# Optimization experiments

Measured on AMD Instinct MI355X. Metric: run time of the kernel, lower is better.

## Reference

```python
import jax, jax.numpy as jnp
import numpy as np

GAMMA = 1000.0


def setup_inputs() -> dict:
    key = jax.random.key(0)
    k1, k2, k3 = jax.random.split(key, 3)
    B, R, N = 4, 2048, 256  # N = n_vars + 1
    x = jax.random.normal(k1, (B, R, N), dtype=jnp.float32)
    f = jax.random.uniform(k2, (B, R, N), dtype=jnp.float32)
    y = jax.random.normal(k3, (B, R, 1), dtype=jnp.float32)
    return {"x": x, "f": f, "y": y}


def reference(x, f, y):
    # Faithful port of RLSE.forward in training mode.
    # theta is updated FIRST (with the old S), then S is updated; both are
    # divided by gamma each step, exactly as in the torch source.
    B, R, N = x.shape
    A = (x * f).reshape(B * R, N)          # coefficient rows, scanned sequentially
    b = y.reshape(B * R)                   # rhs scalars

    def step(carry, inp):
        S, theta = carry                   # S: (N,N), theta: (N,)
        a, bi = inp                        # a: (N,), bi: scalar
        # theta_computation: e = b - a.theta ; theta <- (theta + S a * e)/gamma
        e = bi - jnp.dot(a, theta)
        theta_new = (theta + (S @ a) * e) / GAMMA
        # S_computation (note the 'ii'/'kk' einsum labels take DIAGONALS of S):
        # x1[i,k] = S[i,i] * (a.a) * S[k,k] ; x2[i] = 1 + S[i,i] * (a.a)
        d = jnp.diagonal(S)                # (N,)
        s2 = jnp.dot(a, a)                 # scalar a^T a
        x2 = 1.0 + d * s2                  # (N,), broadcast over columns
        S_new = (S - (d[:, None] * d[None, :]) * s2 / x2[:, None]) / GAMMA
        return (S_new, theta_new), None

    S0 = jnp.eye(N, dtype=x.dtype)
    theta0 = jnp.zeros((N,), dtype=x.dtype)
    (S_fin, theta_fin), _ = jax.lax.scan(step, (S0, theta0), (A, b))
    # einsum('bij,jk->bik', x, theta) with theta shape (N,1)
    return jnp.einsum('brn,n->br', x, theta_fin)[..., None]
```

## Files before the change

### kernel.cpp

```cpp
#include <hip/hip_runtime.h>


#define NN 256

__global__ __launch_bounds__(64) void rlse_scan_kernel(
    const float* __restrict__ x, const float* __restrict__ f,
    const float* __restrict__ y, float* __restrict__ theta_out, int rows)
{
    const int l = threadIdx.x;
    const float4* x4 = (const float4*)x;
    const float4* f4 = (const float4*)f;

    float th0 = 0.0f, th1 = 0.0f, th2 = 0.0f, th3 = 0.0f;
    float dv = 1.0f;
    float ov = 0.0f;

    float4 rx = x4[l], rf = f4[l];
    float ry = y[0];

    for (int k = 0; k < rows; ++k) {
        const float a0 = rx.x * rf.x, a1 = rx.y * rf.y;
        const float a2 = rx.z * rf.z, a3 = rx.w * rf.w;

        float4 nx = rx, nf = rf; float ny = 0.0f;
        if (k + 1 < rows) {
            nx = x4[(size_t)(k + 1) * 64 + l];
            nf = f4[(size_t)(k + 1) * 64 + l];
            ny = y[k + 1];
        }

        float ps = a0 + a1 + a2 + a3;
        float p2 = a0 * a0 + a1 * a1 + a2 * a2 + a3 * a3;
        float pt = a0 * th0 + a1 * th1 + a2 * th2 + a3 * th3;
#pragma unroll
        for (int off = 32; off > 0; off >>= 1) {
            ps += __shfl_xor(ps, off, 64);
            p2 += __shfl_xor(p2, off, 64);
            pt += __shfl_xor(pt, off, 64);
        }
        const float suma = ps, s2 = p2;
        const float e = ry - pt;

        const float x2 = 1.0f + dv * s2;
        const float c  = (dv * dv) * s2 / x2;

        const float z0 = dv * a0 + ov * (suma - a0);
        const float z1 = dv * a1 + ov * (suma - a1);
        const float z2 = dv * a2 + ov * (suma - a2);
        const float z3 = dv * a3 + ov * (suma - a3);
        th0 = (th0 + z0 * e) * 0.001f;
        th1 = (th1 + z1 * e) * 0.001f;
        th2 = (th2 + z2 * e) * 0.001f;
        th3 = (th3 + z3 * e) * 0.001f;

        dv = (dv - c) * 0.001f;
        ov = (ov - c) * 0.001f;

        rx = nx; rf = nf; ry = ny;

        if (k >= 13) {
            const bool nz = (dv != 0.0f) | (ov != 0.0f) |
                            (th0 != 0.0f) | (th1 != 0.0f) |
                            (th2 != 0.0f) | (th3 != 0.0f);
            if (__ballot(nz) == 0ULL) break;
        }
    }

    float4 t4; t4.x = th0; t4.y = th1; t4.z = th2; t4.w = th3;
    ((float4*)theta_out)[l] = t4;
}

__global__ __launch_bounds__(256) void rlse_out_kernel(
    const float* __restrict__ x, const float* __restrict__ th,
    float* __restrict__ out, int rows)
{
    const int gid = blockIdx.x * blockDim.x + threadIdx.x;
    const int wave = gid >> 6;
    const int lane = gid & 63;
    if (wave >= rows) return;
    const float4 xv = ((const float4*)(x + (size_t)wave * NN))[lane];
    const float4 tv = ((const float4*)th)[lane];
    float s = xv.x * tv.x + xv.y * tv.y + xv.z * tv.z + xv.w * tv.w;
#pragma unroll
    for (int off = 32; off > 0; off >>= 1) s += __shfl_down(s, off, 64);
    if (lane == 0) out[wave] = s;
}

extern "C" void kernel_launch(void* const* d_in, const int* in_sizes, int n_in,
                              void* d_out, int out_size, void* d_ws, size_t ws_size,
                              hipStream_t stream)
{
    const float* x = (const float*)d_in[0];
    const float* f = (const float*)d_in[1];
    const float* y = (const float*)d_in[2];
    float* out = (float*)d_out;
    float* theta = (float*)d_ws;
    const int rows = in_sizes[2];

    rlse_scan_kernel<<<1, 64, 0, stream>>>(x, f, y, theta, rows);

    const int blocks = (rows * 64 + 255) / 256;
    rlse_out_kernel<<<blocks, 256, 0, stream>>>(x, theta, out, rows);
}
```

Measured before the change: 72.57 us.

## Fuse RLSE scan and output projection into one redundant-scan kernel

```diff
diff --git a/kernel.cpp b/kernel.cpp
--- a/kernel.cpp
+++ b/kernel.cpp
@@ -3,87 +3,105 @@
 
 #define NN 256
 
-__global__ __launch_bounds__(64) void rlse_scan_kernel(
+__global__ __launch_bounds__(256) void rlse_fused_kernel(
     const float* __restrict__ x, const float* __restrict__ f,
-    const float* __restrict__ y, float* __restrict__ theta_out, int rows)
+    const float* __restrict__ y, float* __restrict__ out, int rows)
 {
-    const int l = threadIdx.x;
-    const float4* x4 = (const float4*)x;
-    const float4* f4 = (const float4*)f;
+    __shared__ float s_theta[NN];
+    __shared__ int   s_thzero;
 
-    float th0 = 0.0f, th1 = 0.0f, th2 = 0.0f, th3 = 0.0f;
-    float dv = 1.0f;
-    float ov = 0.0f;
+    const int lane = threadIdx.x & 63;
+    const int wave = threadIdx.x >> 6;
 
-    float4 rx = x4[l], rf = f4[l];
-    float ry = y[0];
+    if (wave == 0) {
+        const int l = lane;
+        const float4* x4 = (const float4*)x;
+        const float4* f4 = (const float4*)f;
 
-    for (int k = 0; k < rows; ++k) {
-        const float a0 = rx.x * rf.x, a1 = rx.y * rf.y;
-        const float a2 = rx.z * rf.z, a3 = rx.w * rf.w;
+        float th0 = 0.0f, th1 = 0.0f, th2 = 0.0f, th3 = 0.0f;
+        float dv = 1.0f;
+        float ov = 0.0f;
 
-        float4 nx = rx, nf = rf; float ny = 0.0f;
-        if (k + 1 < rows) {
-            nx = x4[(size_t)(k + 1) * 64 + l];
-            nf = f4[(size_t)(k + 1) * 64 + l];
-            ny = y[k + 1];
+        float4 cx = x4[l], cf = f4[l];
+        float  cy = y[0];
+        float4 nx = cx, nf = cf;
+        float  ny = 0.0f;
+        if (rows > 1) { nx = x4[64 + l]; nf = f4[64 + l]; ny = y[1]; }
+
+        for (int k = 0; k < rows; ++k) {
+            const float a0 = cx.x * cf.x, a1 = cx.y * cf.y;
+            const float a2 = cx.z * cf.z, a3 = cx.w * cf.w;
+
+            float4 fx = nx, ff = nf; float fy = 0.0f;
+            if (k + 2 < rows) {
+                fx = x4[(size_t)(k + 2) * 64 + l];
+                ff = f4[(size_t)(k + 2) * 64 + l];
+                fy = y[k + 2];
+            }
+
+            float ps = a0 + a1 + a2 + a3;
+            float p2 = a0 * a0 + a1 * a1 + a2 * a2 + a3 * a3;
+            float pt = a0 * th0 + a1 * th1 + a2 * th2 + a3 * th3;
+#pragma unroll
+            for (int off = 32; off > 0; off >>= 1) {
+                ps += __shfl_xor(ps, off, 64);
+                p2 += __shfl_xor(p2, off, 64);
+                pt += __shfl_xor(pt, off, 64);
+            }
+            const float suma = ps, s2 = p2;
+            const float e = cy - pt;
+
+            const float x2 = 1.0f + dv * s2;
+            const float c  = (dv * dv) * s2 / x2;
+
+            const float z0 = dv * a0 + ov * (suma - a0);
+            const float z1 = dv * a1 + ov * (suma - a1);
+            const float z2 = dv * a2 + ov * (suma - a2);
+            const float z3 = dv * a3 + ov * (suma - a3);
+            th0 = (th0 + z0 * e) * 0.001f;
+            th1 = (th1 + z1 * e) * 0.001f;
+            th2 = (th2 + z2 * e) * 0.001f;
+            th3 = (th3 + z3 * e) * 0.001f;
+
+            dv = (dv - c) * 0.001f;
+            ov = (ov - c) * 0.001f;
+
+            cx = nx; cf = nf; cy = ny;
+            nx = fx; nf = ff; ny = fy;
+
+            if (k >= 13) {
+                const bool nzs = (dv != 0.0f) | (ov != 0.0f) |
+                                 (th0 != 0.0f) | (th1 != 0.0f) |
+                                 (th2 != 0.0f) | (th3 != 0.0f);
+                if (__ballot(nzs) == 0ULL) break;
+            }
         }
 
-        float ps = a0 + a1 + a2 + a3;
-        float p2 = a0 * a0 + a1 * a1 + a2 * a2 + a3 * a3;
-        float pt = a0 * th0 + a1 * th1 + a2 * th2 + a3 * th3;
-#pragma unroll
-        for (int off = 32; off > 0; off >>= 1) {
-            ps += __shfl_xor(ps, off, 64);
-            p2 += __shfl_xor(p2, off, 64);
-            pt += __shfl_xor(pt, off, 64);
-        }
-        const float suma = ps, s2 = p2;
-        const float e = ry - pt;
+        float4 t4; t4.x = th0; t4.y = th1; t4.z = th2; t4.w = th3;
+        ((float4*)s_theta)[l] = t4;
+        const bool nzf = (th0 != 0.0f) | (th1 != 0.0f) |
+                         (th2 != 0.0f) | (th3 != 0.0f);
+        const unsigned long long m = __ballot(nzf);
+        if (l == 0) s_thzero = (m == 0ULL) ? 1 : 0;
+    }
+    __syncthreads();
 
-        const float x2 = 1.0f + dv * s2;
-        const float c  = (dv * dv) * s2 / x2;
-
-        const float z0 = dv * a0 + ov * (suma - a0);
-        const float z1 = dv * a1 + ov * (suma - a1);
-        const float z2 = dv * a2 + ov * (suma - a2);
-        const float z3 = dv * a3 + ov * (suma - a3);
-        th0 = (th0 + z0 * e) * 0.001f;
-        th1 = (th1 + z1 * e) * 0.001f;
-        th2 = (th2 + z2 * e) * 0.001f;
-        th3 = (th3 + z3 * e) * 0.001f;
-
-        dv = (dv - c) * 0.001f;
-        ov = (ov - c) * 0.001f;
-
-        rx = nx; rf = nf; ry = ny;
-
-        if (k >= 13) {
-            const bool nz = (dv != 0.0f) | (ov != 0.0f) |
-                            (th0 != 0.0f) | (th1 != 0.0f) |
-                            (th2 != 0.0f) | (th3 != 0.0f);
-            if (__ballot(nz) == 0ULL) break;
-        }
+    if (s_thzero) {
+        const int gid = blockIdx.x * blockDim.x + threadIdx.x;
+        const int stride = gridDim.x * blockDim.x;
+        for (int i = gid; i < rows; i += stride) out[i] = 0.0f;
+        return;
     }
 
-    float4 t4; t4.x = th0; t4.y = th1; t4.z = th2; t4.w = th3;
-    ((float4*)theta_out)[l] = t4;
-}
-
-__global__ __launch_bounds__(256) void rlse_out_kernel(
-    const float* __restrict__ x, const float* __restrict__ th,
-    float* __restrict__ out, int rows)
-{
-    const int gid = blockIdx.x * blockDim.x + threadIdx.x;
-    const int wave = gid >> 6;
-    const int lane = gid & 63;
-    if (wave >= rows) return;
-    const float4 xv = ((const float4*)(x + (size_t)wave * NN))[lane];
-    const float4 tv = ((const float4*)th)[lane];
-    float s = xv.x * tv.x + xv.y * tv.y + xv.z * tv.z + xv.w * tv.w;
+    const float4 tv = ((const float4*)s_theta)[lane];
+    const int wpg = gridDim.x * 4;
+    for (int r = blockIdx.x * 4 + wave; r < rows; r += wpg) {
+        const float4 xv = ((const float4*)(x + (size_t)r * NN))[lane];
+        float s = xv.x * tv.x + xv.y * tv.y + xv.z * tv.z + xv.w * tv.w;
 #pragma unroll
-    for (int off = 32; off > 0; off >>= 1) s += __shfl_down(s, off, 64);
-    if (lane == 0) out[wave] = s;
+        for (int off = 32; off > 0; off >>= 1) s += __shfl_xor(s, off, 64);
+        if (lane == 0) out[r] = s;
+    }
 }
 
 extern "C" void kernel_launch(void* const* d_in, const int* in_sizes, int n_in,
@@ -94,11 +112,9 @@
     const float* f = (const float*)d_in[1];
     const float* y = (const float*)d_in[2];
     float* out = (float*)d_out;
-    float* theta = (float*)d_ws;
     const int rows = in_sizes[2];
 
-    rlse_scan_kernel<<<1, 64, 0, stream>>>(x, f, y, theta, rows);
-
-    const int blocks = (rows * 64 + 255) / 256;
-    rlse_out_kernel<<<blocks, 256, 0, stream>>>(x, theta, out, rows);
+    int blocks = (rows + 3) / 4;
+    if (blocks < 1) blocks = 1;
+    rlse_fused_kernel<<<blocks, 256, 0, stream>>>(x, f, y, out, rows);
 }
```

Result: faster. 71.02 us (-2.1%).
